# Kernel optimization log

Hardware: AMD Instinct MI355X
Metric: run time of the kernel (lower is better)

Reference implementation:

```python
import jax, jax.numpy as jnp
import numpy as np
import math

HEADS = 8
EMBED = 512
HEAD_DIM = EMBED // HEADS
N, L = 2, 256


def setup_inputs() -> dict:
    key = jax.random.key(0)
    ks = jax.random.split(key, 16)
    s = 0.05  # weight scale for numerical stability
    inp = {
        "values": jax.random.normal(ks[0], (N, L, EMBED), jnp.float32),
        "keys": jax.random.normal(ks[1], (N, L, EMBED), jnp.float32),
        "query": jax.random.normal(ks[2], (N, L, EMBED), jnp.float32),
        "pos": jax.random.normal(ks[3], (N, L, EMBED), jnp.float32),
        "rel": jax.random.normal(ks[4], (N, L, L, EMBED), jnp.float32),
        "mask": jnp.ones((N, L), jnp.float32),
        "Wv": jax.random.normal(ks[5], (HEAD_DIM, HEAD_DIM), jnp.float32) * s,
        "Wk": jax.random.normal(ks[6], (HEAD_DIM, HEAD_DIM), jnp.float32) * s,
        "Wq": jax.random.normal(ks[7], (HEAD_DIM, HEAD_DIM), jnp.float32) * s,
        "Wpq": jax.random.normal(ks[8], (HEAD_DIM, HEAD_DIM), jnp.float32) * s,
        "Wpk": jax.random.normal(ks[9], (HEAD_DIM, HEAD_DIM), jnp.float32) * s,
        "Wrk": jax.random.normal(ks[10], (HEAD_DIM, HEAD_DIM), jnp.float32) * s,
        "Wrq": jax.random.normal(ks[11], (HEAD_DIM, HEAD_DIM), jnp.float32) * s,
        "Wout": jax.random.normal(ks[12], (EMBED, EMBED), jnp.float32) * s,
        "bout": jnp.zeros((EMBED,), jnp.float32),
    }
    return inp


def reference(values, keys, query, pos, rel, mask, Wv, Wk, Wq, Wpq, Wpk, Wrk, Wrq, Wout, bout):
    n, lq, e = query.shape
    h, d = HEADS, e // HEADS
    # split heads; per-head Linear shares one [d,d] weight (y = x @ W.T)
    v = values.reshape(n, -1, h, d) @ Wv.T
    k = keys.reshape(n, -1, h, d) @ Wk.T
    q = query.reshape(n, lq, h, d) @ Wq.T
    p = pos.reshape(n, lq, h, d)
    r = rel.reshape(n, lq, lq, h, d)
    # mode == 'all': QK + pos-pos + two relative terms
    scores = jnp.einsum('nqhd,nkhd->nhqk', q, k)
    pq = p @ Wpq.T
    pk = p @ Wpk.T
    pos_scores = jnp.einsum('nqhd,nkhd->nhqk', pq, pk)
    rk = r @ Wrk.T
    rq = r @ Wrq.T
    rel1 = jnp.einsum('nqhd,nqkhd->nhqk', q, rk)
    rel2 = jnp.einsum('nqkhd,nkhd->nhqk', rq, k)
    energy = (scores + pos_scores + rel1 + rel2) / math.sqrt(2.0)
    energy = energy + (1.0 - mask)[:, None, None, :] * (-1e9)
    attn = jax.nn.softmax(energy, axis=3)
    out = jnp.einsum('nhqk,nkhd->nqhd', attn, v).reshape(n, lq, e)
    return out @ Wout.T + bout
```

## Files before the change

kernel.cpp:

```cpp
#include <hip/hip_runtime.h>
#include <hip/hip_bf16.h>

#define NB 2
#define L 256
#define H 8
#define D 64
#define E 512
#define NL (NB * L)
#define RSQRT2 0.70710678118654752f

__global__ __launch_bounds__(256) void k0_transpose(const float* __restrict__ Wout,
                                                    float* __restrict__ WoutT) {
    __shared__ float tile[64][65];
    int t = threadIdx.x;
    int bi = blockIdx.x >> 3;
    int bj = blockIdx.x & 7;
    int tx = t & 63, ty = t >> 6;
#pragma unroll
    for (int m = 0; m < 16; m++) {
        int el = ty + (m << 2);
        tile[el][tx] = Wout[(size_t)(bi * 64 + el) * E + bj * 64 + tx];
    }
    __syncthreads();
#pragma unroll
    for (int m = 0; m < 16; m++) {
        int cl = ty + (m << 2);
        WoutT[(size_t)(bj * 64 + cl) * E + bi * 64 + tx] = tile[tx][cl];
    }
}

__device__ __forceinline__ float dot64(const float* __restrict__ a,
                                       const float* __restrict__ w) {
    const float4* a4 = (const float4*)a;
    const float4* w4 = (const float4*)w;
    float acc = 0.f;
#pragma unroll
    for (int j = 0; j < 16; j++) {
        float4 x = a4[j], y = w4[j];
        acc = fmaf(x.x, y.x, acc);
        acc = fmaf(x.y, y.y, acc);
        acc = fmaf(x.z, y.z, acc);
        acc = fmaf(x.w, y.w, acc);
    }
    return acc;
}

__global__ __launch_bounds__(256) void k1_proj(
    const float* __restrict__ values, const float* __restrict__ keys,
    const float* __restrict__ query, const float* __restrict__ pos,
    const float* __restrict__ Wv, const float* __restrict__ Wk,
    const float* __restrict__ Wq, const float* __restrict__ Wpq,
    const float* __restrict__ Wpk, const float* __restrict__ Wrk,
    const float* __restrict__ Wrq,
    float* __restrict__ qv_ws, float* __restrict__ kv_ws,
    float* __restrict__ vv_ws, float* __restrict__ pq_ws,
    float* __restrict__ pk_ws, float* __restrict__ qrk_ws,
    float* __restrict__ krq_ws) {
    __shared__ float xq[E], xk[E], xv[E], xp[E];
    __shared__ float qs[E], ks[E];
    int t = threadIdx.x;
    int nl = blockIdx.x;
    size_t base = (size_t)nl * E;
    for (int j = t; j < E; j += 256) {
        xq[j] = query[base + j];
        xk[j] = keys[base + j];
        xv[j] = values[base + j];
        xp[j] = pos[base + j];
    }
    __syncthreads();
#pragma unroll
    for (int cc = 0; cc < 2; cc++) {
        int c = t + cc * 256;
        int h = c >> 6, i = c & 63;
        const float* xqh = xq + (h << 6);
        const float* xkh = xk + (h << 6);
        const float* xvh = xv + (h << 6);
        const float* xph = xp + (h << 6);
        float q_c = dot64(xqh, Wq + (i << 6));
        float k_c = dot64(xkh, Wk + (i << 6));
        float v_c = dot64(xvh, Wv + (i << 6));
        float pq_c = dot64(xph, Wpq + (i << 6));
        float pk_c = dot64(xph, Wpk + (i << 6));
        qv_ws[base + c] = q_c;
        kv_ws[base + c] = k_c;
        vv_ws[base + c] = v_c;
        pq_ws[base + c] = pq_c;
        pk_ws[base + c] = pk_c;
        qs[c] = q_c;
        ks[c] = k_c;
    }
    __syncthreads();
#pragma unroll
    for (int cc = 0; cc < 2; cc++) {
        int c = t + cc * 256;
        int h = c >> 6, d = c & 63;
        float aq = 0.f, ak = 0.f;
        const float* qh = qs + (h << 6);
        const float* kh = ks + (h << 6);
#pragma unroll 8
        for (int i = 0; i < 64; i++) {
            aq = fmaf(qh[i], Wrk[(i << 6) + d], aq);
            ak = fmaf(kh[i], Wrq[(i << 6) + d], ak);
        }
        qrk_ws[base + c] = aq;
        krq_ws[base + c] = ak;
    }
}

__global__ __launch_bounds__(256, 2) void k2a_energy(
    const float* __restrict__ rel, const float* __restrict__ mask,
    const float* __restrict__ qv_ws, const float* __restrict__ kv_ws,
    const float* __restrict__ pq_ws, const float* __restrict__ pk_ws,
    const float* __restrict__ qrk_ws, const float* __restrict__ krq_ws,
    float* __restrict__ e_ws) {
    int t = threadIdx.x;
    int b = blockIdx.x;
    int kc = b & 15;
    int qt = (b >> 4) & 15;
    int n = b >> 8;

    int lane128 = t & 127;
    int rowsel = t >> 7;
    int cq = lane128 << 2;
    int h = lane128 >> 4;
    int sub = t & 15;
    size_t nbase = (size_t)n << 8;
    int kb = kc << 4;

    float4 kq[8], kp[8], pk[8];
    float mk[8];
#pragma unroll
    for (int jj = 0; jj < 8; jj++) {
        int k = kb + (jj << 1) + rowsel;
        kq[jj] = *(const float4*)(krq_ws + (nbase + k) * E + cq);
        kp[jj] = *(const float4*)(kv_ws + (nbase + k) * E + cq);
        pk[jj] = *(const float4*)(pk_ws + (nbase + k) * E + cq);
        mk[jj] = (1.0f - mask[nbase + k]) * (-1e9f);
    }

    for (int qi = 0; qi < 16; qi++) {
        int q = (qt << 4) + qi;
        size_t nq = nbase + q;
        float4 qrk4 = *(const float4*)(qrk_ws + nq * E + cq);
        float4 qv4 = *(const float4*)(qv_ws + nq * E + cq);
        float4 pq4 = *(const float4*)(pq_ws + nq * E + cq);
        const float* relb = rel + nq * (size_t)(L * E);
        float4 r[8];
#pragma unroll
        for (int jj = 0; jj < 8; jj++) {
            int k = kb + (jj << 1) + rowsel;
            r[jj] = *(const float4*)(relb + ((size_t)k << 9) + cq);
        }
        float* eb = e_ws + nq * (H * L);
#pragma unroll
        for (int jj = 0; jj < 8; jj++) {
            float p;
            p = r[jj].x * (qrk4.x + kq[jj].x);
            p = fmaf(r[jj].y, (qrk4.y + kq[jj].y), p);
            p = fmaf(r[jj].z, (qrk4.z + kq[jj].z), p);
            p = fmaf(r[jj].w, (qrk4.w + kq[jj].w), p);
            p = fmaf(kp[jj].x, qv4.x, p);
            p = fmaf(kp[jj].y, qv4.y, p);
            p = fmaf(kp[jj].z, qv4.z, p);
            p = fmaf(kp[jj].w, qv4.w, p);
            p = fmaf(pk[jj].x, pq4.x, p);
            p = fmaf(pk[jj].y, pq4.y, p);
            p = fmaf(pk[jj].z, pq4.z, p);
            p = fmaf(pk[jj].w, pq4.w, p);
            p += __shfl_down(p, 8, 16);
            p += __shfl_down(p, 4, 16);
            p += __shfl_down(p, 2, 16);
            p += __shfl_down(p, 1, 16);
            if (sub == 0) {
                int k = kb + (jj << 1) + rowsel;
                eb[(h << 8) + k] = p * RSQRT2 + mk[jj];
            }
        }
    }
}

__global__ __launch_bounds__(512) void k2b_soft_av(
    const float* __restrict__ e_ws, const float* __restrict__ vv_ws,
    float* __restrict__ attn_ws) {
    __shared__ float e_s[H * L];
    __shared__ float inv_s[H];
    int t = threadIdx.x;
    int nq = blockIdx.x;
    int n = nq >> 8;

    ((float4*)e_s)[t] = ((const float4*)(e_ws + (size_t)nq * (H * L)))[t];
    __syncthreads();

    {
        int hh = t >> 6;
        int lane = t & 63;
        float* eh = e_s + (hh << 8);
        float m = -INFINITY;
#pragma unroll
        for (int j = 0; j < 4; j++) m = fmaxf(m, eh[lane + (j << 6)]);
#pragma unroll
        for (int off = 32; off > 0; off >>= 1) m = fmaxf(m, __shfl_xor(m, off, 64));
        float s = 0.f;
#pragma unroll
        for (int j = 0; j < 4; j++) {
            int idx = lane + (j << 6);
            float ev = __expf(eh[idx] - m);
            eh[idx] = ev;
            s += ev;
        }
#pragma unroll
        for (int off = 32; off > 0; off >>= 1) s += __shfl_xor(s, off, 64);
        if (lane == 0) inv_s[hh] = 1.0f / s;
    }
    __syncthreads();

    {
        int c = t;
        int h1 = t >> 6;
        const float* eh = e_s + (h1 << 8);
        float acc = 0.f;
        const float* vb = vv_ws + (((size_t)n << 8) * E);
#pragma unroll 8
        for (int k = 0; k < L; k++) {
            acc = fmaf(eh[k], vb[((size_t)k << 9) + c], acc);
        }
        attn_ws[(size_t)nq * E + c] = acc * inv_s[h1];
    }
}

__global__ __launch_bounds__(512) void k3_out(const float* __restrict__ attn_ws,
                                              const float* __restrict__ WoutT,
                                              const float* __restrict__ bout,
                                              float* __restrict__ out) {
    __shared__ float As[4 * E];
    int t = threadIdx.x;
    int r0 = blockIdx.x << 2;
    for (int j = t; j < 4 * E; j += 512) As[j] = attn_ws[(size_t)r0 * E + j];
    __syncthreads();
    float b0 = bout[t];
    float a0 = b0, a1 = b0, a2 = b0, a3 = b0;
#pragma unroll 8
    for (int c = 0; c < E; c++) {
        float w = WoutT[((size_t)c << 9) + t];
        a0 = fmaf(As[c], w, a0);
        a1 = fmaf(As[E + c], w, a1);
        a2 = fmaf(As[2 * E + c], w, a2);
        a3 = fmaf(As[3 * E + c], w, a3);
    }
    out[(size_t)(r0 + 0) * E + t] = a0;
    out[(size_t)(r0 + 1) * E + t] = a1;
    out[(size_t)(r0 + 2) * E + t] = a2;
    out[(size_t)(r0 + 3) * E + t] = a3;
}

extern "C" void kernel_launch(void* const* d_in, const int* in_sizes, int n_in,
                              void* d_out, int out_size, void* d_ws, size_t ws_size,
                              hipStream_t stream) {
    const float* values = (const float*)d_in[0];
    const float* keys = (const float*)d_in[1];
    const float* query = (const float*)d_in[2];
    const float* pos = (const float*)d_in[3];
    const float* rel = (const float*)d_in[4];
    const float* mask = (const float*)d_in[5];
    const float* Wv = (const float*)d_in[6];
    const float* Wk = (const float*)d_in[7];
    const float* Wq = (const float*)d_in[8];
    const float* Wpq = (const float*)d_in[9];
    const float* Wpk = (const float*)d_in[10];
    const float* Wrk = (const float*)d_in[11];
    const float* Wrq = (const float*)d_in[12];
    const float* Wout = (const float*)d_in[13];
    const float* bout = (const float*)d_in[14];
    float* out = (float*)d_out;

    float* ws = (float*)d_ws;
    const size_t SZ = (size_t)NL * E;
    float* qv_ws = ws + 0 * SZ;
    float* kv_ws = ws + 1 * SZ;
    float* vv_ws = ws + 2 * SZ;
    float* pq_ws = ws + 3 * SZ;
    float* pk_ws = ws + 4 * SZ;
    float* qrk_ws = ws + 5 * SZ;
    float* krq_ws = ws + 6 * SZ;
    float* attn_ws = ws + 7 * SZ;
    float* WoutT = ws + 8 * SZ;
    float* e_ws = ws + 9 * SZ;

    k0_transpose<<<64, 256, 0, stream>>>(Wout, WoutT);
    k1_proj<<<NL, 256, 0, stream>>>(values, keys, query, pos, Wv, Wk, Wq, Wpq,
                                    Wpk, Wrk, Wrq, qv_ws, kv_ws, vv_ws, pq_ws,
                                    pk_ws, qrk_ws, krq_ws);
    k2a_energy<<<512, 256, 0, stream>>>(rel, mask, qv_ws, kv_ws, pq_ws,
                                        pk_ws, qrk_ws, krq_ws, e_ws);
    k2b_soft_av<<<NL, 512, 0, stream>>>(e_ws, vv_ws, attn_ws);
    k3_out<<<NL / 4, 512, 0, stream>>>(attn_ws, WoutT, bout, out);
}
```

Measured before the change: 490.6 us.

## Split energy kernel into QK/pos pass and software-pipelined rel-streaming pass

The energy kernel is split in two. A small tiled kernel computes the QK and pos-pos scores plus the mask. A separate kernel streams the large rel tensor with a four-deep register prefetch pipeline so loads overlap the reductions. The softmax kernel now adds the two partial energy buffers, and its AV product is split across four key segments with float4 loads and a shared-memory reduction. This trades an extra launch, an extra workspace buffer and more register pressure for better memory-latency hiding on the bandwidth-bound rel read.

Result: slower. 508.6 us (+3.7%).

```diff
diff --git a/kernel.cpp b/kernel.cpp
--- a/kernel.cpp
+++ b/kernel.cpp
@@ -107,12 +107,95 @@
     }
 }
 
-__global__ __launch_bounds__(256, 2) void k2a_energy(
-    const float* __restrict__ rel, const float* __restrict__ mask,
+__global__ __launch_bounds__(256) void k2pre(
     const float* __restrict__ qv_ws, const float* __restrict__ kv_ws,
     const float* __restrict__ pq_ws, const float* __restrict__ pk_ws,
-    const float* __restrict__ qrk_ws, const float* __restrict__ krq_ws,
-    float* __restrict__ e_ws) {
+    const float* __restrict__ mask, float* __restrict__ e_ws) {
+    __shared__ float qs[8 * 64], ps[8 * 64];
+    int t = threadIdx.x;
+    int b = blockIdx.x;
+    int qt = b & 31;
+    int h = (b >> 5) & 7;
+    int n = b >> 8;
+    int nb = n << 8;
+    int q0 = qt << 3;
+    int k = t;
+#pragma unroll
+    for (int it = 0; it < 2; it++) {
+        int idx = t + (it << 8);
+        int q = idx >> 6, d = idx & 63;
+        size_t g = (size_t)(nb + q0 + q) * E + (h << 6) + d;
+        qs[idx] = qv_ws[g];
+        ps[idx] = pq_ws[g];
+    }
+    __syncthreads();
+    const float4* kv4p = (const float4*)(kv_ws + (size_t)(nb + k) * E + (h << 6));
+    const float4* pk4p = (const float4*)(pk_ws + (size_t)(nb + k) * E + (h << 6));
+    float acc[8];
+#pragma unroll
+    for (int q = 0; q < 8; q++) acc[q] = 0.f;
+#pragma unroll
+    for (int d4 = 0; d4 < 16; d4++) {
+        float4 kv4 = kv4p[d4];
+        float4 pk4 = pk4p[d4];
+#pragma unroll
+        for (int q = 0; q < 8; q++) {
+            float4 q4 = ((const float4*)qs)[(q << 4) + d4];
+            float4 p4 = ((const float4*)ps)[(q << 4) + d4];
+            float a = acc[q];
+            a = fmaf(q4.x, kv4.x, a);
+            a = fmaf(q4.y, kv4.y, a);
+            a = fmaf(q4.z, kv4.z, a);
+            a = fmaf(q4.w, kv4.w, a);
+            a = fmaf(p4.x, pk4.x, a);
+            a = fmaf(p4.y, pk4.y, a);
+            a = fmaf(p4.z, pk4.z, a);
+            a = fmaf(p4.w, pk4.w, a);
+            acc[q] = a;
+        }
+    }
+    float mk = (1.0f - mask[nb + k]) * (-1e9f);
+#pragma unroll
+    for (int q = 0; q < 8; q++) {
+        e_ws[(size_t)(nb + q0 + q) * (H * L) + (h << 8) + k] = acc[q] * RSQRT2 + mk;
+    }
+}
+
+
+#define K2REL_LOAD(R, QK, qi_)                                                  \
+    do {                                                                        \
+        const int gq_ = nbase + q0 + (qi_);                                     \
+        const float* relb_ =                                                    \
+            rel + (size_t)gq_ * (size_t)(L * E) + (size_t)kb * E + cq;          \
+        _Pragma("unroll") for (int jj = 0; jj < 8; jj++)                        \
+            R[jj] = *(const float4*)(relb_ + (size_t)((jj << 1) + rowsel) * E); \
+        QK = *(const float4*)(qrk_ws + (size_t)gq_ * E + cq);                   \
+    } while (0)
+
+#define K2REL_COMP(R, QK, qi_)                                                  \
+    do {                                                                        \
+        const int gq_ = nbase + q0 + (qi_);                                     \
+        float* rb_ = r_ws + (size_t)gq_ * (H * L) + (h << 8);                   \
+        _Pragma("unroll") for (int jj = 0; jj < 8; jj++) {                      \
+            float wx = QK.x + kq[jj].x;                                         \
+            float wy = QK.y + kq[jj].y;                                         \
+            float wz = QK.z + kq[jj].z;                                         \
+            float ww = QK.w + kq[jj].w;                                         \
+            float p = R[jj].x * wx;                                             \
+            p = fmaf(R[jj].y, wy, p);                                           \
+            p = fmaf(R[jj].z, wz, p);                                           \
+            p = fmaf(R[jj].w, ww, p);                                           \
+            p += __shfl_down(p, 8, 16);                                         \
+            p += __shfl_down(p, 4, 16);                                         \
+            p += __shfl_down(p, 2, 16);                                         \
+            p += __shfl_down(p, 1, 16);                                         \
+            if (sub == 0) rb_[kb + (jj << 1) + rowsel] = p * RSQRT2;            \
+        }                                                                       \
+    } while (0)
+
+__global__ __launch_bounds__(256, 2) void k2rel(
+    const float* __restrict__ rel, const float* __restrict__ qrk_ws,
+    const float* __restrict__ krq_ws, float* __restrict__ r_ws) {
     int t = threadIdx.x;
     int b = blockIdx.x;
     int kc = b & 15;
@@ -124,71 +207,51 @@
     int cq = lane128 << 2;
     int h = lane128 >> 4;
     int sub = t & 15;
-    size_t nbase = (size_t)n << 8;
+    int nbase = n << 8;
     int kb = kc << 4;
-
-    float4 kq[8], kp[8], pk[8];
-    float mk[8];
+    int q0 = qt << 4;
+
+    float4 kq[8];
 #pragma unroll
     for (int jj = 0; jj < 8; jj++) {
-        int k = kb + (jj << 1) + rowsel;
-        kq[jj] = *(const float4*)(krq_ws + (nbase + k) * E + cq);
-        kp[jj] = *(const float4*)(kv_ws + (nbase + k) * E + cq);
-        pk[jj] = *(const float4*)(pk_ws + (nbase + k) * E + cq);
-        mk[jj] = (1.0f - mask[nbase + k]) * (-1e9f);
-    }
-
-    for (int qi = 0; qi < 16; qi++) {
-        int q = (qt << 4) + qi;
-        size_t nq = nbase + q;
-        float4 qrk4 = *(const float4*)(qrk_ws + nq * E + cq);
-        float4 qv4 = *(const float4*)(qv_ws + nq * E + cq);
-        float4 pq4 = *(const float4*)(pq_ws + nq * E + cq);
-        const float* relb = rel + nq * (size_t)(L * E);
-        float4 r[8];
-#pragma unroll
-        for (int jj = 0; jj < 8; jj++) {
-            int k = kb + (jj << 1) + rowsel;
-            r[jj] = *(const float4*)(relb + ((size_t)k << 9) + cq);
-        }
-        float* eb = e_ws + nq * (H * L);
-#pragma unroll
-        for (int jj = 0; jj < 8; jj++) {
-            float p;
-            p = r[jj].x * (qrk4.x + kq[jj].x);
-            p = fmaf(r[jj].y, (qrk4.y + kq[jj].y), p);
-            p = fmaf(r[jj].z, (qrk4.z + kq[jj].z), p);
-            p = fmaf(r[jj].w, (qrk4.w + kq[jj].w), p);
-            p = fmaf(kp[jj].x, qv4.x, p);
-            p = fmaf(kp[jj].y, qv4.y, p);
-            p = fmaf(kp[jj].z, qv4.z, p);
-            p = fmaf(kp[jj].w, qv4.w, p);
-            p = fmaf(pk[jj].x, pq4.x, p);
-            p = fmaf(pk[jj].y, pq4.y, p);
-            p = fmaf(pk[jj].z, pq4.z, p);
-            p = fmaf(pk[jj].w, pq4.w, p);
-            p += __shfl_down(p, 8, 16);
-            p += __shfl_down(p, 4, 16);
-            p += __shfl_down(p, 2, 16);
-            p += __shfl_down(p, 1, 16);
-            if (sub == 0) {
-                int k = kb + (jj << 1) + rowsel;
-                eb[(h << 8) + k] = p * RSQRT2 + mk[jj];
-            }
-        }
+        kq[jj] = *(const float4*)(krq_ws +
+                                  (size_t)(nbase + kb + (jj << 1) + rowsel) * E + cq);
+    }
+
+    float4 rA[8], rB[8], rC[8], rD[8];
+    float4 qA, qB, qC, qD;
+    K2REL_LOAD(rA, qA, 0);
+    K2REL_LOAD(rB, qB, 1);
+    K2REL_LOAD(rC, qC, 2);
+#pragma unroll
+    for (int qi = 0; qi < 16; qi += 4) {
+        K2REL_LOAD(rD, qD, qi + 3);
+        K2REL_COMP(rA, qA, qi);
+        if (qi < 12) K2REL_LOAD(rA, qA, qi + 4);
+        K2REL_COMP(rB, qB, qi + 1);
+        if (qi < 12) K2REL_LOAD(rB, qB, qi + 5);
+        K2REL_COMP(rC, qC, qi + 2);
+        if (qi < 12) K2REL_LOAD(rC, qC, qi + 6);
+        K2REL_COMP(rD, qD, qi + 3);
     }
 }
 
 __global__ __launch_bounds__(512) void k2b_soft_av(
-    const float* __restrict__ e_ws, const float* __restrict__ vv_ws,
-    float* __restrict__ attn_ws) {
+    const float* __restrict__ e_ws, const float* __restrict__ r_ws,
+    const float* __restrict__ vv_ws, float* __restrict__ attn_ws) {
     __shared__ float e_s[H * L];
+    __shared__ float PS[4 * E];
     __shared__ float inv_s[H];
     int t = threadIdx.x;
     int nq = blockIdx.x;
     int n = nq >> 8;
 
-    ((float4*)e_s)[t] = ((const float4*)(e_ws + (size_t)nq * (H * L)))[t];
+    {
+        float4 a = ((const float4*)(e_ws + (size_t)nq * (H * L)))[t];
+        float4 b = ((const float4*)(r_ws + (size_t)nq * (H * L)))[t];
+        a.x += b.x; a.y += b.y; a.z += b.z; a.w += b.w;
+        ((float4*)e_s)[t] = a;
+    }
     __syncthreads();
 
     {
@@ -215,16 +278,29 @@
     __syncthreads();
 
     {
+        int c4 = (t & 127) << 2;
+        int kseg = t >> 7;
+        int h1 = c4 >> 6;
+        const float* eh = e_s + (h1 << 8) + (kseg << 6);
+        const float* vb = vv_ws + ((size_t)(n << 8) + (kseg << 6)) * E + c4;
+        float4 acc = {0.f, 0.f, 0.f, 0.f};
+#pragma unroll 16
+        for (int k = 0; k < 64; k++) {
+            float ev = eh[k];
+            float4 v4 = *(const float4*)(vb + (size_t)k * E);
+            acc.x = fmaf(ev, v4.x, acc.x);
+            acc.y = fmaf(ev, v4.y, acc.y);
+            acc.z = fmaf(ev, v4.z, acc.z);
+            acc.w = fmaf(ev, v4.w, acc.w);
+        }
+        *(float4*)(PS + kseg * E + c4) = acc;
+    }
+    __syncthreads();
+
+    {
         int c = t;
-        int h1 = t >> 6;
-        const float* eh = e_s + (h1 << 8);
-        float acc = 0.f;
-        const float* vb = vv_ws + (((size_t)n << 8) * E);
-#pragma unroll 8
-        for (int k = 0; k < L; k++) {
-            acc = fmaf(eh[k], vb[((size_t)k << 9) + c], acc);
-        }
-        attn_ws[(size_t)nq * E + c] = acc * inv_s[h1];
+        float v = PS[c] + PS[E + c] + PS[2 * E + c] + PS[3 * E + c];
+        attn_ws[(size_t)nq * E + c] = v * inv_s[t >> 6];
     }
 }
 
@@ -285,13 +361,14 @@
     float* attn_ws = ws + 7 * SZ;
     float* WoutT = ws + 8 * SZ;
     float* e_ws = ws + 9 * SZ;
+    float* r_ws = e_ws + (size_t)NL * (H * L);
 
     k0_transpose<<<64, 256, 0, stream>>>(Wout, WoutT);
     k1_proj<<<NL, 256, 0, stream>>>(values, keys, query, pos, Wv, Wk, Wq, Wpq,
                                     Wpk, Wrk, Wrq, qv_ws, kv_ws, vv_ws, pq_ws,
                                     pk_ws, qrk_ws, krq_ws);
-    k2a_energy<<<512, 256, 0, stream>>>(rel, mask, qv_ws, kv_ws, pq_ws,
-                                        pk_ws, qrk_ws, krq_ws, e_ws);
-    k2b_soft_av<<<NL, 512, 0, stream>>>(e_ws, vv_ws, attn_ws);
+    k2pre<<<512, 256, 0, stream>>>(qv_ws, kv_ws, pq_ws, pk_ws, mask, e_ws);
+    k2rel<<<512, 256, 0, stream>>>(rel, qrk_ws, krq_ws, r_ws);
+    k2b_soft_av<<<NL, 512, 0, stream>>>(e_ws, r_ws, vv_ws, attn_ws);
     k3_out<<<NL / 4, 512, 0, stream>>>(attn_ws, WoutT, bout, out);
 }
```
